# Kernel tuning notes

Measured on AMD Instinct MI355X. Metric: run time of the kernel, lower is better.

The kernel has to match this reference:

```python
import jax, jax.numpy as jnp
import numpy as np

V = 50000
E = 800000
B, FIN, FOUT, K = 2, 64, 64, 4


def setup_inputs() -> dict:
    key = jax.random.key(0)
    k1, k2, k3, k4, k5, k6 = jax.random.split(key, 6)
    inputs = jax.random.normal(k1, (B, V, FIN), dtype=jnp.float32)
    weight = jax.random.normal(k2, (K, FIN, FOUT), dtype=jnp.float32) * np.sqrt(2.0 / (FIN * K)).astype(np.float32)
    bias = jax.random.normal(k3, (FOUT,), dtype=jnp.float32)
    lap_vals = jax.random.normal(k4, (E,), dtype=jnp.float32)
    lap_rows = jax.random.randint(k5, (E,), 0, V, dtype=jnp.int32)
    lap_cols = jax.random.randint(k6, (E,), 0, V, dtype=jnp.int32)
    return {"inputs": inputs, "weight": weight, "bias": bias,
            "lap_vals": lap_vals, "lap_rows": lap_rows, "lap_cols": lap_cols}


def reference(inputs, weight, bias, lap_vals, lap_rows, lap_cols):
    B_, V_, Fin = inputs.shape
    K_, _, Fout = weight.shape

    def spmm(x):  # L @ x, L in COO; x: [V, Fin*B]
        return jax.ops.segment_sum(lap_vals[:, None] * x[lap_cols], lap_rows, num_segments=V_)

    # x0: [V, Fin*B] (Fin-major flatten, matching torch permute(1,2,0).view)
    x0 = jnp.transpose(inputs, (1, 2, 0)).reshape(V_, Fin * B_)
    xs = [x0]
    if K_ > 1:
        x1 = spmm(x0)
        xs.append(x1)
        for _ in range(2, K_):
            x2 = 2.0 * spmm(x1) - x0
            xs.append(x2)
            x0, x1 = x1, x2
    # [K,V,Fin,B] -> [B,V,Fin,K] -> [B*V, Fin*K]
    X = jnp.stack(xs).reshape(K_, V_, Fin, B_)
    X = jnp.transpose(X, (3, 1, 2, 0)).reshape(B_ * V_, Fin * K_)
    # faithful to original: weight flattened as (K*Fin, Fout)
    out = X @ weight.reshape(K_ * Fin, Fout)
    return out.reshape(B_, V_, Fout) + bias
```

## Files before the change

kernel.cpp:

```cpp
#include <hip/hip_runtime.h>
#include <hip/hip_bf16.h>


#define NV 50000
#define NE 800000
#define XROW 128
#define NROWS 100000
#define NTILES 6250
#define EPMAX 1600000
#define BSHIFT 7
#define RPB 128
#define NB 391
#define CAP 3072
#define CHUNK 4096
#define P1_BLOCKS 196
#define X0_BLOCKS 12500

using u16 = unsigned short;
using u32 = unsigned int;
using u64 = unsigned long long;
typedef __bf16 bf16x8 __attribute__((ext_vector_type(8)));
typedef float f32x4 __attribute__((ext_vector_type(4)));

__device__ __forceinline__ float bflo(u32 g) { return __uint_as_float(g << 16); }
__device__ __forceinline__ float bfhi(u32 g) { return __uint_as_float(g & 0xffff0000u); }
__device__ __forceinline__ u32 pack_bf2(float a, float b) {
    u16 ha = __builtin_bit_cast(u16, (__bf16)a);
    u16 hb = __builtin_bit_cast(u16, (__bf16)b);
    return (u32)ha | ((u32)hb << 16);
}
__device__ __forceinline__ float unpack_f16hi(u32 rec) {
    u16 h = (u16)(rec >> 16);
    return (float)__builtin_bit_cast(_Float16, h);
}
__device__ __forceinline__ int pad16(int n) { return (n + 15) & ~15; }

__global__ __launch_bounds__(256) void bin1_k(const int* __restrict__ rows, const int* __restrict__ cols,
                                              const float* __restrict__ vals,
                                              int* __restrict__ binctr, u64* __restrict__ tmp) {
    __shared__ int bcnt[NB];
    __shared__ int bofs[NB];
    __shared__ int bcur[NB];
    __shared__ int gbase[NB];
    __shared__ int ps[256];
    __shared__ u64 stage[CHUNK];
    int t = threadIdx.x;
    int base = blockIdx.x * CHUNK;
    int n = NE - base;
    if (n > CHUNK) n = CHUNK;
    if (n <= 0) return;

    for (int i = t; i < NB; i += 256) bcnt[i] = 0;
    __syncthreads();

    for (int i = t; i < n; i += 256) {
        atomicAdd(&bcnt[rows[base + i] >> BSHIFT], 1);
    }
    __syncthreads();

    int i0 = 2 * t, i1 = 2 * t + 1;
    int a0 = (i0 < NB) ? bcnt[i0] : 0;
    int a1 = (i1 < NB) ? bcnt[i1] : 0;
    ps[t] = a0 + a1;
    __syncthreads();
    for (int off = 1; off < 256; off <<= 1) {
        int v = (t >= off) ? ps[t - off] : 0;
        __syncthreads();
        ps[t] += v;
        __syncthreads();
    }
    int eb = ps[t] - (a0 + a1);
    if (i0 < NB) { bofs[i0] = eb;      bcur[i0] = eb;      gbase[i0] = i0 * CAP + atomicAdd(&binctr[i0], a0); }
    if (i1 < NB) { bofs[i1] = eb + a0; bcur[i1] = eb + a0; gbase[i1] = i1 * CAP + atomicAdd(&binctr[i1], a1); }
    __syncthreads();

    for (int i = t; i < n; i += 256) {
        int r = rows[base + i];
        int c = cols[base + i];
        u16 hv = __builtin_bit_cast(u16, (_Float16)vals[base + i]);
        u64 rec = ((u64)(u32)r << 32) | (u64)((u32)c | ((u32)hv << 16));
        int s = atomicAdd(&bcur[r >> BSHIFT], 1);
        stage[s] = rec;
    }
    __syncthreads();

    for (int i = t; i < n; i += 256) {
        u64 rec = stage[i];
        int b = (int)(rec >> (32 + BSHIFT));
        tmp[(size_t)(gbase[b] + (i - bofs[b]))] = rec;
    }
}

__global__ __launch_bounds__(256) void bcnt_k(const u64* __restrict__ tmp, const int* __restrict__ binctr,
                                              int* __restrict__ rowc, int* __restrict__ btot,
                                              int* __restrict__ done,
                                              int* __restrict__ bbase, int* __restrict__ row_ptr) {
    __shared__ int rc[RPB];
    __shared__ int rs[RPB];
    __shared__ int ps[256];
    __shared__ int flag;
    int b = blockIdx.x, t = threadIdx.x;
    int n = binctr[b];
    const u64* rec = tmp + (size_t)b * CAP;
    if (t < RPB) rc[t] = 0;
    __syncthreads();
    for (int i = t; i < n; i += 256) {
        atomicAdd(&rc[(int)(rec[i] >> 32) & (RPB - 1)], 1);
    }
    __syncthreads();
    if (t < RPB) {
        rowc[b * RPB + t] = rc[t];
        rs[t] = pad16(rc[t]);
    }
    __syncthreads();
    for (int off = 64; off > 0; off >>= 1) {
        if (t < off) rs[t] += rs[t + off];
        __syncthreads();
    }
    if (t == 0) {
        btot[b] = rs[0];
        __threadfence();
        int ticket = atomicAdd(done, 1);
        flag = (ticket == NB - 1);
    }
    __syncthreads();
    if (flag) {
        __threadfence();
        int i0 = 2 * t, i1 = 2 * t + 1;
        int a0 = (i0 < NB) ? atomicAdd(&btot[i0], 0) : 0;
        int a1 = (i1 < NB) ? atomicAdd(&btot[i1], 0) : 0;
        ps[t] = a0 + a1;
        __syncthreads();
        for (int off = 1; off < 256; off <<= 1) {
            int v = (t >= off) ? ps[t - off] : 0;
            __syncthreads();
            ps[t] += v;
            __syncthreads();
        }
        int eb = ps[t] - (a0 + a1);
        if (i0 < NB) bbase[i0] = eb;
        if (i1 < NB) bbase[i1] = eb + a0;
        if (t == 255) row_ptr[NV] = ps[255];
    }
}

__global__ __launch_bounds__(256) void place_k(const u64* __restrict__ tmp, const int* __restrict__ binctr,
                                               const int* __restrict__ rowc, const int* __restrict__ bbase,
                                               int* __restrict__ row_ptr, u32* __restrict__ epack) {
    __shared__ int rc[RPB];
    __shared__ int ro[RPB];
    int b = blockIdx.x, t = threadIdx.x;
    int n = binctr[b];
    int base = bbase[b];
    const u64* rec = tmp + (size_t)b * CAP;

    int cv = (t < RPB) ? rowc[b * RPB + t] : 0;
    int pv = pad16(cv);
    if (t < RPB) ro[t] = pv;
    __syncthreads();
    for (int off = 1; off < RPB; off <<= 1) {
        int v = 0;
        if (t < RPB && t >= off) v = ro[t - off];
        __syncthreads();
        if (t < RPB) ro[t] += v;
        __syncthreads();
    }
    if (t < RPB) {
        int ex = ro[t] - pv;
        ro[t] = ex;
        rc[t] = 0;
        int v = (b << BSHIFT) + t;
        if (v < NV) row_ptr[v] = base + ex;
    }
    __syncthreads();
    for (int i = t; i < n; i += 256) {
        u64 r64 = rec[i];
        int r = (int)(r64 >> 32) & (RPB - 1);
        int p = base + ro[r] + atomicAdd(&rc[r], 1);
        epack[p] = (u32)r64;
    }
    __syncthreads();
    if (t < RPB) {
        int s = base + ro[t] + cv;
        int e = base + ro[t] + pv;
        for (int i = s; i < e; ++i) epack[i] = 0;
    }
}

__global__ void bx0w_k(const float* __restrict__ in, u32* __restrict__ x0u,
                       const float* __restrict__ weight, u16* __restrict__ wimg) {
    int bid = blockIdx.x;
    if (bid < X0_BLOCKS) {
        int i = bid * 256 + threadIdx.x;
        int v = i >> 6, p = i & 63;
        int b = p >> 5;
        int f = (p & 31) * 2;
        const float* src = in + (size_t)b * (NV * 64) + (size_t)v * 64 + f;
        float2 t = *(const float2*)src;
        x0u[i] = pack_bf2(t.x, t.y);
    } else {
        int i = (bid - X0_BLOCKS) * 256 + threadIdx.x;
        int c = i >> 6, o = i & 63;
        int cp = ((c & 3) << 6) | (c >> 2);
        wimg[o * 264 + cp] = __builtin_bit_cast(u16, (__bf16)weight[i]);
    }
}

__global__ __launch_bounds__(256) void spmm_k(const u32* __restrict__ x,
                                              const u32* __restrict__ xprev,
                                              const int* __restrict__ row_ptr,
                                              const u32* __restrict__ epack,
                                              u32* __restrict__ xout, int mode) {
    int wave = (int)((blockIdx.x * blockDim.x + threadIdx.x) >> 6);
    u32 lane = threadIdx.x & 63;
    int row = __builtin_amdgcn_readfirstlane(wave);
    if (row >= NV) return;
    int beg = row_ptr[row];
    int end = row_ptr[row + 1];
    int q = (int)(lane >> 4);
    u32 g16 = lane & 15;

    float ax[4] = {0.f, 0.f, 0.f, 0.f};
    float ay[4] = {0.f, 0.f, 0.f, 0.f};

    for (int e = beg; e < end; e += 16) {
        uint4 r4 = *(const uint4*)(epack + e + 4 * q);
        u32 rec[4] = {r4.x, r4.y, r4.z, r4.w};
        uint4 gv[4];
        #pragma unroll
        for (int u = 0; u < 4; ++u)
            gv[u] = *(const uint4*)(x + ((rec[u] & 0xffffu) << 6) + (g16 << 2));
        #pragma unroll
        for (int u = 0; u < 4; ++u) {
            float w = unpack_f16hi(rec[u]);
            ax[0] += w * bflo(gv[u].x); ay[0] += w * bfhi(gv[u].x);
            ax[1] += w * bflo(gv[u].y); ay[1] += w * bfhi(gv[u].y);
            ax[2] += w * bflo(gv[u].z); ay[2] += w * bfhi(gv[u].z);
            ax[3] += w * bflo(gv[u].w); ay[3] += w * bfhi(gv[u].w);
        }
    }

    #pragma unroll
    for (int m = 16; m <= 32; m <<= 1) {
        #pragma unroll
        for (int j = 0; j < 4; ++j) {
            ax[j] += __shfl_xor(ax[j], m, 64);
            ay[j] += __shfl_xor(ay[j], m, 64);
        }
    }

    if (q == 0) {
        if (mode) {
            uint4 pv = *(const uint4*)(xprev + ((u32)row << 6) + (g16 << 2));
            ax[0] = 2.f * ax[0] - bflo(pv.x); ay[0] = 2.f * ay[0] - bfhi(pv.x);
            ax[1] = 2.f * ax[1] - bflo(pv.y); ay[1] = 2.f * ay[1] - bfhi(pv.y);
            ax[2] = 2.f * ax[2] - bflo(pv.z); ay[2] = 2.f * ay[2] - bfhi(pv.z);
            ax[3] = 2.f * ax[3] - bflo(pv.w); ay[3] = 2.f * ay[3] - bfhi(pv.w);
        }
        uint4 o;
        o.x = pack_bf2(ax[0], ay[0]);
        o.y = pack_bf2(ax[1], ay[1]);
        o.z = pack_bf2(ax[2], ay[2]);
        o.w = pack_bf2(ax[3], ay[3]);
        *(uint4*)(xout + ((u32)row << 6) + (g16 << 2)) = o;
    }
}

__global__ __launch_bounds__(512) void spmm3f_k(const u32* __restrict__ x2,
                                                const u32* __restrict__ x1,
                                                const int* __restrict__ row_ptr,
                                                const u32* __restrict__ epack,
                                                const u16* __restrict__ x_all,
                                                const u16* __restrict__ wimg,
                                                const float* __restrict__ bias,
                                                float* __restrict__ out) {
    __shared__ u32 As[4 * 8 * 64];
    int t0 = blockIdx.x;
    int tid = threadIdx.x;
    int w = tid >> 6;
    u32 lane = tid & 63;

    #pragma unroll
    for (int k = 0; k < 3; ++k) {
        int i = tid + k * 512;
        int arr = i >> 9;
        int vp = (i >> 6) & 7;
        int c = i & 63;
        u32 val = *((const u32*)x_all + ((size_t)arr * NV + (size_t)(t0 * 8 + vp)) * 64 + c);
        int unit = (c >> 2) ^ (vp & 7);
        As[(arr * 8 + vp) * 64 + unit * 4 + (c & 3)] = val;
    }

    {
        int row = __builtin_amdgcn_readfirstlane(t0 * 8 + w);
        int beg = row_ptr[row];
        int end = row_ptr[row + 1];
        int q = (int)(lane >> 4);
        u32 g16 = lane & 15;

        float ax[4] = {0.f, 0.f, 0.f, 0.f};
        float ay[4] = {0.f, 0.f, 0.f, 0.f};

        for (int e = beg; e < end; e += 16) {
            uint4 r4 = *(const uint4*)(epack + e + 4 * q);
            u32 rec[4] = {r4.x, r4.y, r4.z, r4.w};
            uint4 gv[4];
            #pragma unroll
            for (int u = 0; u < 4; ++u)
                gv[u] = *(const uint4*)(x2 + ((rec[u] & 0xffffu) << 6) + (g16 << 2));
            #pragma unroll
            for (int u = 0; u < 4; ++u) {
                float wgt = unpack_f16hi(rec[u]);
                ax[0] += wgt * bflo(gv[u].x); ay[0] += wgt * bfhi(gv[u].x);
                ax[1] += wgt * bflo(gv[u].y); ay[1] += wgt * bfhi(gv[u].y);
                ax[2] += wgt * bflo(gv[u].z); ay[2] += wgt * bfhi(gv[u].z);
                ax[3] += wgt * bflo(gv[u].w); ay[3] += wgt * bfhi(gv[u].w);
            }
        }

        #pragma unroll
        for (int m = 16; m <= 32; m <<= 1) {
            #pragma unroll
            for (int j = 0; j < 4; ++j) {
                ax[j] += __shfl_xor(ax[j], m, 64);
                ay[j] += __shfl_xor(ay[j], m, 64);
            }
        }

        if (q == 0) {
            uint4 pv = *(const uint4*)(x1 + ((u32)row << 6) + (g16 << 2));
            ax[0] = 2.f * ax[0] - bflo(pv.x); ay[0] = 2.f * ay[0] - bfhi(pv.x);
            ax[1] = 2.f * ax[1] - bflo(pv.y); ay[1] = 2.f * ay[1] - bfhi(pv.y);
            ax[2] = 2.f * ax[2] - bflo(pv.z); ay[2] = 2.f * ay[2] - bfhi(pv.z);
            ax[3] = 2.f * ax[3] - bflo(pv.w); ay[3] = 2.f * ay[3] - bfhi(pv.w);
            int unit = (int)g16 ^ (w & 7);
            u32* dst = &As[(3 * 8 + w) * 64 + unit * 4];
            dst[0] = pack_bf2(ax[0], ay[0]);
            dst[1] = pack_bf2(ax[1], ay[1]);
            dst[2] = pack_bf2(ax[2], ay[2]);
            dst[3] = pack_bf2(ax[3], ay[3]);
        }
    }
    __syncthreads();

    if (w < 4) {
        int j = w;
        int m = (int)lane & 15;
        int q8 = ((int)lane >> 4) * 8;
        int vp = m >> 1;
        int b = m & 1;
        f32x4 acc = {0, 0, 0, 0};
        #pragma unroll
        for (int kb = 0; kb < 8; ++kb) {
            int arr = kb >> 1;
            int unit = (b * 8 + (kb & 1) * 4 + ((int)lane >> 4)) ^ (vp & 7);
            bf16x8 a = *(const bf16x8*)&As[(arr * 8 + vp) * 64 + unit * 4];
            bf16x8 bj = *(const bf16x8*)&wimg[(j * 16 + m) * 264 + kb * 32 + q8];
            acc = __builtin_amdgcn_mfma_f32_16x16x32_bf16(a, bj, acc, 0, 0, 0);
        }
        float bv = bias[j * 16 + m];
        int rbase = t0 * 16 + ((int)lane >> 4) * 4;
        #pragma unroll
        for (int reg = 0; reg < 4; ++reg) {
            int rr = rbase + reg;
            out[(size_t)(rr & 1) * (NV * 64) + (size_t)(rr >> 1) * 64 + j * 16 + m] = acc[reg] + bv;
        }
    }
}

extern "C" void kernel_launch(void* const* d_in, const int* in_sizes, int n_in,
                              void* d_out, int out_size, void* d_ws, size_t ws_size,
                              hipStream_t stream) {
    const float* inputs = (const float*)d_in[0];
    const float* weight = (const float*)d_in[1];
    const float* bias   = (const float*)d_in[2];
    const float* lapv   = (const float*)d_in[3];
    const int*   lrows  = (const int*)d_in[4];
    const int*   lcols  = (const int*)d_in[5];
    float* out = (float*)d_out;

    char* ws = (char*)d_ws;
    size_t o = 0;
    auto alloc = [&](size_t bytes) -> void* {
        void* p = ws + o;
        o += (bytes + 255) & ~(size_t)255;
        return p;
    };
    u16* x_all = (u16*)alloc((size_t)4 * NV * XROW * 2);
    u32* epack = (u32*)alloc((size_t)EPMAX * 4);
    u64* tmp   = (u64*)alloc((size_t)NB * CAP * 8);
    int* row_ptr = (int*)alloc((size_t)(NV + 1) * 4);
    int* binctr  = (int*)alloc((size_t)(NB + 1) * 4);
    int* btot    = (int*)alloc((size_t)NB * 4);
    int* bbase   = (int*)alloc((size_t)NB * 4);
    int* rowc    = (int*)alloc((size_t)NB * RPB * 4);
    u16* wimg = (u16*)alloc((size_t)64 * 264 * 2);
    (void)ws_size; (void)in_sizes; (void)n_in; (void)out_size;

    int* done = binctr + NB;

    u32* x0 = (u32*)(x_all + (size_t)0 * NV * XROW);
    u32* x1 = (u32*)(x_all + (size_t)1 * NV * XROW);
    u32* x2 = (u32*)(x_all + (size_t)2 * NV * XROW);

    hipMemsetAsync(binctr, 0, (size_t)(NB + 1) * 4, stream);
    bin1_k<<<P1_BLOCKS, 256, 0, stream>>>(lrows, lcols, lapv, binctr, tmp);
    bcnt_k<<<NB, 256, 0, stream>>>(tmp, binctr, rowc, btot, done, bbase, row_ptr);
    place_k<<<NB, 256, 0, stream>>>(tmp, binctr, rowc, bbase, row_ptr, epack);
    bx0w_k<<<X0_BLOCKS + 64, 256, 0, stream>>>(inputs, x0, weight, wimg);

    spmm_k<<<(NV + 3) / 4, 256, 0, stream>>>(x0, nullptr, row_ptr, epack, x1, 0);
    spmm_k<<<(NV + 3) / 4, 256, 0, stream>>>(x1, x0, row_ptr, epack, x2, 1);

    spmm3f_k<<<NTILES, 512, 0, stream>>>(x2, x1, row_ptr, epack, x_all, wimg, bias, out);
}
```

Measured before the change: 227.5 us.

## Split each SpMM row across four blocks by feature quarter

Restructures the two SpMM kernels so each row is handled by four waves in different blocks, each covering one quarter of the 128 features, with 16 edge slots per wave instead of 4. This raises the launch from about 12.5k to 50k blocks and gives more parallel gathers per edge chunk, aiming to improve latency hiding on the irregular gather. In exchange the edge records are read four times, shuffle reductions get longer, and each gather is narrower (64 bytes per row segment).

```diff
diff --git a/kernel.cpp b/kernel.cpp
--- a/kernel.cpp
+++ b/kernel.cpp
@@ -206,42 +206,38 @@
     }
 }
 
-__global__ __launch_bounds__(256) void spmm_k(const u32* __restrict__ x,
-                                              const u32* __restrict__ xprev,
-                                              const int* __restrict__ row_ptr,
-                                              const u32* __restrict__ epack,
-                                              u32* __restrict__ xout, int mode) {
-    int wave = (int)((blockIdx.x * blockDim.x + threadIdx.x) >> 6);
+__global__ __launch_bounds__(256) void spmmq_k(const u32* __restrict__ x,
+                                               const u32* __restrict__ xprev,
+                                               const int* __restrict__ row_ptr,
+                                               const u32* __restrict__ epack,
+                                               u32* __restrict__ xout, int mode) {
+    int b = blockIdx.x;
+    int quarter = b & 3;
+    int w = threadIdx.x >> 6;
+    int row = (b >> 2) * 4 + w;
     u32 lane = threadIdx.x & 63;
-    int row = __builtin_amdgcn_readfirstlane(wave);
-    if (row >= NV) return;
+    int slot = (int)(lane >> 2);
+    u32 g4 = lane & 3;
+    u32 qbase = (u32)quarter * 16 + (g4 << 2);
+
     int beg = row_ptr[row];
     int end = row_ptr[row + 1];
-    int q = (int)(lane >> 4);
-    u32 g16 = lane & 15;
 
     float ax[4] = {0.f, 0.f, 0.f, 0.f};
     float ay[4] = {0.f, 0.f, 0.f, 0.f};
 
     for (int e = beg; e < end; e += 16) {
-        uint4 r4 = *(const uint4*)(epack + e + 4 * q);
-        u32 rec[4] = {r4.x, r4.y, r4.z, r4.w};
-        uint4 gv[4];
-        #pragma unroll
-        for (int u = 0; u < 4; ++u)
-            gv[u] = *(const uint4*)(x + ((rec[u] & 0xffffu) << 6) + (g16 << 2));
-        #pragma unroll
-        for (int u = 0; u < 4; ++u) {
-            float w = unpack_f16hi(rec[u]);
-            ax[0] += w * bflo(gv[u].x); ay[0] += w * bfhi(gv[u].x);
-            ax[1] += w * bflo(gv[u].y); ay[1] += w * bfhi(gv[u].y);
-            ax[2] += w * bflo(gv[u].z); ay[2] += w * bfhi(gv[u].z);
-            ax[3] += w * bflo(gv[u].w); ay[3] += w * bfhi(gv[u].w);
-        }
+        u32 rec = epack[e + slot];
+        uint4 gv = *(const uint4*)(x + ((rec & 0xffffu) << 6) + qbase);
+        float wgt = unpack_f16hi(rec);
+        ax[0] += wgt * bflo(gv.x); ay[0] += wgt * bfhi(gv.x);
+        ax[1] += wgt * bflo(gv.y); ay[1] += wgt * bfhi(gv.y);
+        ax[2] += wgt * bflo(gv.z); ay[2] += wgt * bfhi(gv.z);
+        ax[3] += wgt * bflo(gv.w); ay[3] += wgt * bfhi(gv.w);
     }
 
     #pragma unroll
-    for (int m = 16; m <= 32; m <<= 1) {
+    for (int m = 4; m <= 32; m <<= 1) {
         #pragma unroll
         for (int j = 0; j < 4; ++j) {
             ax[j] += __shfl_xor(ax[j], m, 64);
@@ -249,9 +245,9 @@
         }
     }
 
-    if (q == 0) {
+    if (slot == 0) {
         if (mode) {
-            uint4 pv = *(const uint4*)(xprev + ((u32)row << 6) + (g16 << 2));
+            uint4 pv = *(const uint4*)(xprev + ((u32)row << 6) + qbase);
             ax[0] = 2.f * ax[0] - bflo(pv.x); ay[0] = 2.f * ay[0] - bfhi(pv.x);
             ax[1] = 2.f * ax[1] - bflo(pv.y); ay[1] = 2.f * ay[1] - bfhi(pv.y);
             ax[2] = 2.f * ax[2] - bflo(pv.z); ay[2] = 2.f * ay[2] - bfhi(pv.z);
@@ -262,7 +258,7 @@
         o.y = pack_bf2(ax[1], ay[1]);
         o.z = pack_bf2(ax[2], ay[2]);
         o.w = pack_bf2(ax[3], ay[3]);
-        *(uint4*)(xout + ((u32)row << 6) + (g16 << 2)) = o;
+        *(uint4*)(xout + ((u32)row << 6) + qbase) = o;
     }
 }
 
@@ -409,8 +405,8 @@
     place_k<<<NB, 256, 0, stream>>>(tmp, binctr, rowc, bbase, row_ptr, epack);
     bx0w_k<<<X0_BLOCKS + 64, 256, 0, stream>>>(inputs, x0, weight, wimg);
 
-    spmm_k<<<(NV + 3) / 4, 256, 0, stream>>>(x0, nullptr, row_ptr, epack, x1, 0);
-    spmm_k<<<(NV + 3) / 4, 256, 0, stream>>>(x1, x0, row_ptr, epack, x2, 1);
+    spmmq_k<<<NV, 256, 0, stream>>>(x0, nullptr, row_ptr, epack, x1, 0);
+    spmmq_k<<<NV, 256, 0, stream>>>(x1, x0, row_ptr, epack, x2, 1);
 
     spmm3f_k<<<NTILES, 512, 0, stream>>>(x2, x1, row_ptr, epack, x_all, wimg, bias, out);
 }
```

Measured after the change: 313.7 us. +37.9%, slower.
